# Kernel tuning notes

Hardware: AMD Instinct MI355X
Metric: run time of the kernel (lower is better)

The kernel has to match this reference:

```python
import jax, jax.numpy as jnp
import numpy as np
import math

N_HEADS = 32
N_KV_HEADS = 8
MAX_SEQ_LEN = 2048


def _rope_cos_sin(seq_len, head_dim, dtype):
    # precompute_freqs_cis: theta=10000, positions 0..seq_len-1 (note: NOT offset by start_pos, faithful to source)
    inv_freq = 1.0 / (10000.0 ** (jnp.arange(0, head_dim, 2, dtype=jnp.float32) / head_dim))
    t = jnp.arange(seq_len, dtype=jnp.float32)
    angles = jnp.outer(t, inv_freq)  # [S, hd/2]
    return jnp.cos(angles).astype(dtype), jnp.sin(angles).astype(dtype)


def _apply_rope(x, cos, sin):
    # x: [B, S, H, hd]; rotate consecutive pairs (llama complex convention)
    B, S, H, hd = x.shape
    xr = x.reshape(B, S, H, hd // 2, 2)
    x1, x2 = xr[..., 0], xr[..., 1]
    c = cos[None, :, None, :]
    s = sin[None, :, None, :]
    o1 = x1 * c - x2 * s
    o2 = x1 * s + x2 * c
    return jnp.stack([o1, o2], axis=-1).reshape(B, S, H, hd)


def setup_inputs() -> dict:
    key = jax.random.key(0)
    ks = jax.random.split(key, 5)
    dim = 4096
    B, S = 1, 2048
    sd = 1.0 / math.sqrt(dim)
    return {
        "x": jax.random.normal(ks[0], (B, S, dim), dtype=jnp.float32),
        "wq": jax.random.normal(ks[1], (4096, 4096), dtype=jnp.float32) * sd,
        "wk": jax.random.normal(ks[2], (1024, 4096), dtype=jnp.float32) * sd,
        "wv": jax.random.normal(ks[3], (1024, 4096), dtype=jnp.float32) * sd,
        "wo": jax.random.normal(ks[4], (4096, 4096), dtype=jnp.float32) * sd,
        "start_pos": 0,
    }


def reference(x, wq, wk, wv, wo, start_pos):
    B, S, D = x.shape
    Hq, Hkv = N_HEADS, N_KV_HEADS
    hd = D // Hq
    n_rep = Hq // Hkv

    xq = (x @ wq.T).reshape(B, S, Hq, hd)
    xk = (x @ wk.T).reshape(B, S, Hkv, hd)
    xv = (x @ wv.T).reshape(B, S, Hkv, hd)

    cos, sin = _rope_cos_sin(S, hd, x.dtype)
    xq = _apply_rope(xq, cos, sin)
    xk = _apply_rope(xk, cos, sin)

    # KV cache append + read back [:, :start_pos+S] (start_pos is a static Python int)
    cache_k = jnp.zeros((B, MAX_SEQ_LEN, Hkv, hd), dtype=x.dtype)
    cache_v = jnp.zeros((B, MAX_SEQ_LEN, Hkv, hd), dtype=x.dtype)
    cache_k = jax.lax.dynamic_update_slice(cache_k, xk, (0, start_pos, 0, 0))
    cache_v = jax.lax.dynamic_update_slice(cache_v, xv, (0, start_pos, 0, 0))
    kv_len = start_pos + S
    keys = cache_k[:, :kv_len]    # [B, K, Hkv, hd]
    values = cache_v[:, :kv_len]

    # GQA repeat_kv: [B, K, Hkv, hd] -> [B, K, Hq, hd]
    keys = jnp.broadcast_to(keys[:, :, :, None, :], (B, kv_len, Hkv, n_rep, hd)).reshape(B, kv_len, Hq, hd)
    values = jnp.broadcast_to(values[:, :, :, None, :], (B, kv_len, Hkv, n_rep, hd)).reshape(B, kv_len, Hq, hd)

    scale = 1.0 / math.sqrt(hd)
    scores = jnp.einsum('bqhd,bkhd->bhqk', xq, keys) * scale  # [B, Hq, S, K]
    # NOTE: source applies NO causal mask — faithful reproduction
    attn = jax.nn.softmax(scores, axis=-1)
    out = jnp.einsum('bhqk,bkhd->bqhd', attn, values).reshape(B, S, Hq * hd)
    return out @ wo.T
```

## Files before the change

### kernel.cpp

```cpp
#include <hip/hip_runtime.h>
#include <hip/hip_bf16.h>

typedef __bf16 bf16_t;
typedef _Float16 f16_t;
typedef unsigned int uint;
typedef __attribute__((ext_vector_type(8))) __bf16 bf16x8;
typedef __attribute__((ext_vector_type(4))) __bf16 bf16x4;
typedef __attribute__((ext_vector_type(8))) _Float16 f16x8;
typedef __attribute__((ext_vector_type(4))) _Float16 f16x4;
typedef __attribute__((ext_vector_type(4))) float f32x4;
typedef __attribute__((ext_vector_type(16))) float f32x16;

__global__ __launch_bounds__(256) void repack_x16(const float* __restrict__ src,
                                                  uint16_t* __restrict__ dh)
{
    const int p  = blockIdx.y;
    const int kb = blockIdx.x;
    const int tid = threadIdx.x;
    const int rr = tid >> 3;
    const int k4 = tid & 7;
    const int slot = k4 >> 1;
    const int so   = (k4 & 1) * 4;
    uint16_t* bh = dh + ((size_t)p * 128 + kb) * 4096;
    #pragma unroll
    for (int it = 0; it < 4; ++it) {
        const int r = it * 32 + rr;
        const float4 v = *reinterpret_cast<const float4*>(
            &src[((size_t)p * 128 + r) * 4096 + kb * 32 + k4 * 4]);
        float f[4] = {v.x, v.y, v.z, v.w};
        f16x4 h;
        #pragma unroll
        for (int e = 0; e < 4; ++e) h[e] = (f16_t)f[e];
        const int pos = r * 32 + ((slot ^ ((r >> 1) & 3)) << 3) + so;
        *reinterpret_cast<f16x4*>(&bh[pos]) = h;
    }
}

__global__ __launch_bounds__(256) void repack_w96_16(const float* __restrict__ wq,
                                                     const float* __restrict__ wk,
                                                     const float* __restrict__ wv,
                                                     uint16_t* __restrict__ dst)
{
    const int kb  = blockIdx.x;
    const int pan = blockIdx.y;
    const int tid = threadIdx.x;
    const int k4 = tid & 7;
    const int slot = k4 >> 1;
    const int so   = (k4 & 1) * 4;
    uint16_t* bh = dst + ((size_t)pan * 128 + kb) * 3072;
    #pragma unroll
    for (int it = 0; it < 3; ++it) {
        const int r = it * 32 + (tid >> 3);
        const int n = pan * 96 + r;
        const float* srow = (n < 4096) ? (wq + (size_t)n * 4096)
                          : (n < 5120) ? (wk + (size_t)(n - 4096) * 4096)
                                       : (wv + (size_t)(n - 5120) * 4096);
        const float4 v = *reinterpret_cast<const float4*>(srow + kb * 32 + k4 * 4);
        float f[4] = {v.x, v.y, v.z, v.w};
        f16x4 h;
        #pragma unroll
        for (int e = 0; e < 4; ++e) h[e] = (f16_t)f[e];
        const int pos = r * 32 + ((slot ^ ((r >> 1) & 3)) << 3) + so;
        *reinterpret_cast<f16x4*>(&bh[pos]) = h;
    }
}

__global__ __launch_bounds__(256) void repack_h16(const float* __restrict__ src,
                                                  uint16_t* __restrict__ dh)
{
    const int p  = blockIdx.y;
    const int kb = blockIdx.x;
    const int tid = threadIdx.x;
    const int rr = tid >> 3;
    const int k4 = tid & 7;
    const int slot = k4 >> 1;
    const int so   = (k4 & 1) * 4;
    uint16_t* bh = dh + ((size_t)p * 128 + kb) * 4096;
    #pragma unroll
    for (int it = 0; it < 4; ++it) {
        const int r = it * 32 + rr;
        const float4 v = *reinterpret_cast<const float4*>(
            &src[((size_t)p * 128 + r) * 4096 + kb * 32 + k4 * 4]);
        float f[4] = {v.x, v.y, v.z, v.w};
        f16x4 h;
        #pragma unroll
        for (int e = 0; e < 4; ++e) h[e] = (f16_t)f[e];
        const int pos = r * 32 + ((slot ^ ((r >> 1) & 3)) << 3) + so;
        *reinterpret_cast<f16x4*>(&bh[pos]) = h;
    }
}

__global__ __launch_bounds__(512) void gemm_qkv7(const uint16_t* __restrict__ xh,
                                                 const uint16_t* __restrict__ wqkv,
                                                 float* __restrict__ xq,
                                                 float* __restrict__ xk,
                                                 float* __restrict__ xv)
{
    __shared__ char lds[3][28672];

    const int bid = blockIdx.x;
    const int swz = (bid & 7) * 32 + (bid >> 3);
    const int by = swz >> 5;
    const int bx = swz & 31;
    const int tid = threadIdx.x;
    const int w = tid >> 6, lane = tid & 63;
    const int wm = w >> 2, wn = w & 3;
    const int fr = lane & 15, s4 = lane >> 4;

    const int cw = (w < 4) ? 4 : 3;
    const uint16_t* sp[4];
    int dof[4];
    int stridec[4];
    #pragma unroll
    for (int i = 0; i < 4; ++i) {
        const int c = w + 8 * i;
        if (c < 16) {
            sp[i] = xh + (size_t)(2 * by + (c >> 3)) * 524288 + (c & 7) * 512 + lane * 8;
            dof[i] = c * 1024;
            stridec[i] = 4096;
        } else {
            const int cb = (c - 16) % 12;
            sp[i] = wqkv + (size_t)(bx * 2 + (cb >= 6 ? 1 : 0)) * 393216 + (cb % 6) * 512 + lane * 8;
            dof[i] = 16384 + cb * 1024;
            stridec[i] = 3072;
        }
    }

    f32x4 acc[8][3] = {};

    #pragma unroll
    for (int i = 0; i < 4; ++i)
        if (i < cw)
            __builtin_amdgcn_global_load_lds(
                (const __attribute__((address_space(1))) void*)(sp[i]),
                (__attribute__((address_space(3))) void*)(&lds[0][0] + dof[i]), 16, 0, 0);
    #pragma unroll
    for (int i = 0; i < 4; ++i)
        if (i < cw)
            __builtin_amdgcn_global_load_lds(
                (const __attribute__((address_space(1))) void*)(sp[i] + stridec[i]),
                (__attribute__((address_space(3))) void*)(&lds[1][0] + dof[i]), 16, 0, 0);
    if (w < 4) asm volatile("s_waitcnt vmcnt(4)" ::: "memory");
    else       asm volatile("s_waitcnt vmcnt(3)" ::: "memory");
    __builtin_amdgcn_s_barrier();
    __builtin_amdgcn_sched_barrier(0);

    int cur = 0;
    for (int t = 0; t < 128; ++t) {
        if (t + 2 < 128) {
            int nb = cur + 2; if (nb >= 3) nb -= 3;
            #pragma unroll
            for (int i = 0; i < 4; ++i)
                if (i < cw)
                    __builtin_amdgcn_global_load_lds(
                        (const __attribute__((address_space(1))) void*)(sp[i] + (size_t)(t + 2) * stridec[i]),
                        (__attribute__((address_space(3))) void*)(&lds[nb][0] + dof[i]), 16, 0, 0);
        }
        const char* b = &lds[cur][0];

        f16x8 fb[3];
        #pragma unroll
        for (int j = 0; j < 3; ++j) {
            const int cbp = wn * 48 + j * 16 + fr;
            const int pan = (cbp >= 96) ? 1 : 0;
            const int rb = cbp - pan * 96;
            fb[j] = *reinterpret_cast<const f16x8*>(b + 16384 + pan * 6144 + rb * 64 + ((s4 ^ ((rb >> 1) & 3)) << 4));
        }
        #pragma unroll
        for (int p = 0; p < 4; ++p) {
            f16x8 fh[2];
            #pragma unroll
            for (int f = 0; f < 2; ++f) {
                const int rl = wm * 128 + p * 32 + f * 16 + fr;
                fh[f] = *reinterpret_cast<const f16x8*>(b + rl * 64 + ((s4 ^ ((rl >> 1) & 3)) << 4));
            }
            __builtin_amdgcn_s_setprio(1);
            #pragma unroll
            for (int f = 0; f < 2; ++f)
                #pragma unroll
                for (int j = 0; j < 3; ++j)
                    acc[p * 2 + f][j] = __builtin_amdgcn_mfma_f32_16x16x32_f16(fh[f], fb[j], acc[p * 2 + f][j], 0, 0, 0);
            __builtin_amdgcn_s_setprio(0);
        }
        if (t + 2 < 128) {
            if (w < 4) asm volatile("s_waitcnt vmcnt(4)" ::: "memory");
            else       asm volatile("s_waitcnt vmcnt(3)" ::: "memory");
        } else {
            asm volatile("s_waitcnt vmcnt(0)" ::: "memory");
        }
        __builtin_amdgcn_s_barrier();
        __builtin_amdgcn_sched_barrier(0);
        if (++cur == 3) cur = 0;
    }

    const int r0 = by * 256 + wm * 128 + s4 * 4;
    const int c0 = bx * 192 + wn * 48 + fr;
    #pragma unroll
    for (int ri = 0; ri < 8; ++ri)
        #pragma unroll
        for (int j = 0; j < 3; ++j) {
            const int col = c0 + j * 16;
            #pragma unroll
            for (int rr = 0; rr < 4; ++rr) {
                const int row = r0 + ri * 16 + rr;
                if (col < 4096)      xq[(size_t)row * 4096 + col] = acc[ri][j][rr];
                else if (col < 5120) xk[(size_t)row * 1024 + (col - 4096)] = acc[ri][j][rr];
                else                 xv[(size_t)row * 1024 + (col - 5120)] = acc[ri][j][rr];
            }
        }
}

__global__ __launch_bounds__(512) void gemm_out7(const uint16_t* __restrict__ aoh,
                                                 const uint16_t* __restrict__ woh,
                                                 float* __restrict__ out)
{
    __shared__ char lds[3][24576];

    const int bid = blockIdx.x;
    const int swz = (bid & 7) * 32 + (bid >> 3);
    const int by = swz >> 5;
    const int bx = swz & 31;
    const int tid = threadIdx.x;
    const int w = tid >> 6, lane = tid & 63;
    const int wm = w >> 2, wn = w & 3;
    const int fr = lane & 15, s4 = lane >> 4;

    const uint16_t* sp[3];
    int dof[3];
    #pragma unroll
    for (int i = 0; i < 3; ++i) {
        const int c = w + 8 * i;
        if (c < 16) {
            sp[i]  = aoh + (size_t)(2 * by + (c >> 3)) * 524288 + (c & 7) * 512 + lane * 8;
            dof[i] = c * 1024;
        } else {
            sp[i]  = woh + (size_t)bx * 524288 + (c - 16) * 512 + lane * 8;
            dof[i] = 16384 + (c - 16) * 1024;
        }
    }

    f32x4 acc[8][2] = {};

    #pragma unroll
    for (int i = 0; i < 3; ++i)
        __builtin_amdgcn_global_load_lds(
            (const __attribute__((address_space(1))) void*)(sp[i]),
            (__attribute__((address_space(3))) void*)(&lds[0][0] + dof[i]), 16, 0, 0);
    #pragma unroll
    for (int i = 0; i < 3; ++i)
        __builtin_amdgcn_global_load_lds(
            (const __attribute__((address_space(1))) void*)(sp[i] + 4096),
            (__attribute__((address_space(3))) void*)(&lds[1][0] + dof[i]), 16, 0, 0);
    asm volatile("s_waitcnt vmcnt(3)" ::: "memory");
    __builtin_amdgcn_s_barrier();
    __builtin_amdgcn_sched_barrier(0);

    int cur = 0;
    for (int t = 0; t < 128; ++t) {
        if (t + 2 < 128) {
            int nb = cur + 2; if (nb >= 3) nb -= 3;
            #pragma unroll
            for (int i = 0; i < 3; ++i)
                __builtin_amdgcn_global_load_lds(
                    (const __attribute__((address_space(1))) void*)(sp[i] + (size_t)(t + 2) * 4096),
                    (__attribute__((address_space(3))) void*)(&lds[nb][0] + dof[i]), 16, 0, 0);
        }
        const char* b = &lds[cur][0];

        f16x8 fb[2];
        #pragma unroll
        for (int j = 0; j < 2; ++j) {
            const int cbp = wn * 32 + j * 16 + fr;
            fb[j] = *reinterpret_cast<const f16x8*>(b + 16384 + cbp * 64 + ((s4 ^ ((cbp >> 1) & 3)) << 4));
        }
        #pragma unroll
        for (int p = 0; p < 4; ++p) {
            f16x8 fh[2];
            #pragma unroll
            for (int f = 0; f < 2; ++f) {
                const int rl = p * 32 + f * 16 + fr;
                fh[f] = *reinterpret_cast<const f16x8*>(b + wm * 8192 + rl * 64 + ((s4 ^ ((rl >> 1) & 3)) << 4));
            }
            __builtin_amdgcn_s_setprio(1);
            #pragma unroll
            for (int f = 0; f < 2; ++f)
                #pragma unroll
                for (int j = 0; j < 2; ++j)
                    acc[p * 2 + f][j] = __builtin_amdgcn_mfma_f32_16x16x32_f16(fh[f], fb[j], acc[p * 2 + f][j], 0, 0, 0);
            __builtin_amdgcn_s_setprio(0);
        }
        if (t + 2 < 128) asm volatile("s_waitcnt vmcnt(3)" ::: "memory");
        else             asm volatile("s_waitcnt vmcnt(0)" ::: "memory");
        __builtin_amdgcn_s_barrier();
        __builtin_amdgcn_sched_barrier(0);
        if (++cur == 3) cur = 0;
    }

    const int r0 = by * 256 + wm * 128 + s4 * 4;
    const int c0 = bx * 128 + wn * 32 + fr;
    #pragma unroll
    for (int ri = 0; ri < 8; ++ri)
        #pragma unroll
        for (int j = 0; j < 2; ++j)
            #pragma unroll
            for (int rr = 0; rr < 4; ++rr)
                out[(size_t)(r0 + ri * 16 + rr) * 4096 + c0 + j * 16] = acc[ri][j][rr];
}

__global__ __launch_bounds__(256) void rope_k(float* __restrict__ xq, float* __restrict__ xk)
{
    const int idx = blockIdx.x * 256 + threadIdx.x;
    const int TOTQ = 2048 * 32 * 64;
    int s, j;
    float* base;
    bool isq = idx < TOTQ;
    if (isq) {
        s = idx >> 11;
        const int rem = idx & 2047;
        j = rem & 63;
        base = xq + (size_t)s * 4096 + (rem >> 6) * 128 + 2 * j;
    } else {
        const int i2 = idx - TOTQ;
        s = i2 >> 9;
        const int rem = i2 & 511;
        j = rem & 63;
        base = xk + (size_t)s * 1024 + (rem >> 6) * 128 + 2 * j;
    }
    const float invf = exp2f(-(float)j * (13.287712379549449f / 64.0f));
    const float ang = (float)s * invf;
    float sn, cs;
    sincosf(ang, &sn, &cs);
    float2 v = *reinterpret_cast<float2*>(base);
    float2 r;
    r.x = v.x * cs - v.y * sn;
    r.y = v.x * sn + v.y * cs;
    if (isq) { r.x *= 0.08838834764831845f; r.y *= 0.08838834764831845f; }
    *reinterpret_cast<float2*>(base) = r;
}

__global__ __launch_bounds__(256) void conv_kv(const float* __restrict__ xk,
                                               const float* __restrict__ xv,
                                               uint16_t* __restrict__ kvg)
{
    __shared__ float V[32][129];
    const int t = blockIdx.x;
    const int h = blockIdx.y;
    const int tid = threadIdx.x;
    uint16_t* tile = kvg + ((size_t)(h * 64 + t)) * 12288;

    #pragma unroll
    for (int i = 0; i < 4; ++i) {
        int v = i * 256 + tid;
        int row = v >> 5, c4 = (v & 31) * 4;
        *reinterpret_cast<float4*>(&V[row][c4]) =
            *reinterpret_cast<const float4*>(&xv[(size_t)(t * 32 + row) * 1024 + h * 128 + c4]);
    }

    {
        const int r = tid >> 3;
        const int d0 = (tid & 7) * 16;
        float f[16];
        const float* kr = &xk[(size_t)(t * 32 + r) * 1024 + h * 128 + d0];
        *reinterpret_cast<float4*>(&f[0])  = *reinterpret_cast<const float4*>(kr);
        *reinterpret_cast<float4*>(&f[4])  = *reinterpret_cast<const float4*>(kr + 4);
        *reinterpret_cast<float4*>(&f[8])  = *reinterpret_cast<const float4*>(kr + 8);
        *reinterpret_cast<float4*>(&f[12]) = *reinterpret_cast<const float4*>(kr + 12);
        #pragma unroll
        for (int cc = 0; cc < 2; ++cc) {
            bf16x8 hv, lv;
            #pragma unroll
            for (int e = 0; e < 8; ++e) {
                float x = f[cc * 8 + e];
                bf16_t hb = (bf16_t)x;
                hv[e] = hb;
                lv[e] = (bf16_t)(x - (float)hb);
            }
            const int c = (d0 >> 3) + cc;
            const int pos = r * 128 + ((c ^ (r & 15)) << 3);
            *reinterpret_cast<bf16x8*>(&tile[pos]) = hv;
            *reinterpret_cast<bf16x8*>(&tile[4096 + pos]) = lv;
        }
    }
    __syncthreads();
    {
        const int d = tid >> 1;
        const int k0 = (tid & 1) * 16;
        float g[16];
        #pragma unroll
        for (int j = 0; j < 16; ++j) g[j] = V[k0 + j][d];
        #pragma unroll
        for (int cc = 0; cc < 2; ++cc) {
            bf16x8 hv;
            #pragma unroll
            for (int e = 0; e < 8; ++e) hv[e] = (bf16_t)g[cc * 8 + e];
            const int c = (k0 >> 3) + cc;
            const int pos = d * 32 + ((c ^ (d & 3)) << 3);
            *reinterpret_cast<bf16x8*>(&tile[8192 + pos]) = hv;
        }
    }
}

__device__ __forceinline__ uint cvtpk(float lo, float hi) {
    uint r;
    asm("v_cvt_pk_bf16_f32 %0, %1, %2" : "=v"(r) : "v"(lo), "v"(hi));
    return r;
}
__device__ __forceinline__ void permswap(uint& a, uint& b) {
    asm("v_permlane32_swap_b32 %0, %1" : "+v"(a), "+v"(b));
}
__device__ __forceinline__ bf16x8 pack4(uint w0, uint w1, uint w2, uint w3) {
    union { uint u[4]; bf16x8 v; } t;
    t.u[0] = w0; t.u[1] = w1; t.u[2] = w2; t.u[3] = w3;
    return t.v;
}

__global__ __launch_bounds__(512, 2) void attn_mfma(const float* __restrict__ xq,
                                                    const uint16_t* __restrict__ kvg,
                                                    uint16_t* __restrict__ aoh)
{
    __shared__ char lds[2][24576];

    const int b = blockIdx.x;
    const int kvh = b & 7;
    const int r = b >> 3;
    const int h = kvh * 4 + (r & 3);
    const int q0 = (r >> 2) * 256;
    const int tid = threadIdx.x;
    const int w = tid >> 6;
    const int lane = tid & 63;
    const int ln31 = lane & 31;
    const int hi = lane >> 5;

    const int q = q0 + w * 32 + ln31;
    const float* qrow = xq + (size_t)q * 4096 + h * 128;
    bf16x8 Qh[8];
    #pragma unroll
    for (int ks = 0; ks < 8; ++ks) {
        float f[8];
        *reinterpret_cast<float4*>(&f[0]) = *reinterpret_cast<const float4*>(qrow + ks * 16 + hi * 8);
        *reinterpret_cast<float4*>(&f[4]) = *reinterpret_cast<const float4*>(qrow + ks * 16 + hi * 8 + 4);
        #pragma unroll
        for (int e = 0; e < 8; ++e) Qh[ks][e] = (bf16_t)f[e];
    }

    const char* gkv = (const char*)kvg + (size_t)kvh * 64 * 24576;

    f32x16 oacc[4] = {{}, {}, {}, {}};
    float m = -3.0e38f, l = 0.f;

    {
        #pragma unroll
        for (int i = 0; i < 3; ++i) {
            const int chunk = i * 8 + w;
            __builtin_amdgcn_global_load_lds(
                (const __attribute__((address_space(1))) void*)(gkv + chunk * 1024 + lane * 16),
                (__attribute__((address_space(3))) void*)(&lds[0][chunk * 1024]),
                16, 0, 0);
        }
    }

    for (int t = 0; t < 64; ++t) {
        __syncthreads();
        if (t + 1 < 64) {
            const char* g = gkv + (size_t)(t + 1) * 24576;
            const int buf = (t + 1) & 1;
            #pragma unroll
            for (int i = 0; i < 3; ++i) {
                const int chunk = i * 8 + w;
                __builtin_amdgcn_global_load_lds(
                    (const __attribute__((address_space(1))) void*)(g + chunk * 1024 + lane * 16),
                    (__attribute__((address_space(3))) void*)(&lds[buf][chunk * 1024]),
                    16, 0, 0);
            }
        }
        const int cur = t & 1;
        const char* Kh = lds[cur];
        const char* Kl = lds[cur] + 8192;
        const char* Vh = lds[cur] + 16384;

        f32x16 s0 = {}, s1 = {};
        __builtin_amdgcn_s_setprio(1);
        #pragma unroll
        for (int ks = 0; ks < 8; ++ks) {
            const int byt = ln31 * 256 + ((ks * 32 + hi * 16) ^ ((ln31 & 15) << 4));
            bf16x8 ah = *reinterpret_cast<const bf16x8*>(Kh + byt);
            bf16x8 al = *reinterpret_cast<const bf16x8*>(Kl + byt);
            s0 = __builtin_amdgcn_mfma_f32_32x32x16_bf16(ah, Qh[ks], s0, 0, 0, 0);
            s1 = __builtin_amdgcn_mfma_f32_32x32x16_bf16(al, Qh[ks], s1, 0, 0, 0);
        }
        __builtin_amdgcn_s_setprio(0);
        f32x16 s = s0 + s1;

        float pmax = s[0];
        #pragma unroll
        for (int jj = 1; jj < 16; ++jj) pmax = fmaxf(pmax, s[jj]);
        pmax = fmaxf(pmax, __shfl_xor(pmax, 32));
        if (!__all(pmax - m <= 8.0f)) {
            const float mnew = fmaxf(m, pmax);
            const float corr = __expf(m - mnew);
            l *= corr;
            #pragma unroll
            for (int dt = 0; dt < 4; ++dt) oacc[dt] *= corr;
            m = mnew;
        }
        float psum = 0.f;
        #pragma unroll
        for (int jj = 0; jj < 16; ++jj) {
            float pv = __expf(s[jj] - m);
            s[jj] = pv;
            psum += pv;
        }
        psum += __shfl_xor(psum, 32);
        l += psum;

        #pragma unroll
        for (int ks = 0; ks < 2; ++ks) {
            const int b0 = ks * 8;
            uint wa = cvtpk(s[b0 + 0], s[b0 + 1]);
            uint wb = cvtpk(s[b0 + 2], s[b0 + 3]);
            uint wc = cvtpk(s[b0 + 4], s[b0 + 5]);
            uint wd = cvtpk(s[b0 + 6], s[b0 + 7]);
            permswap(wa, wc); permswap(wb, wd);
            bf16x8 Pf = pack4(wa, wb, wc, wd);
            __builtin_amdgcn_s_setprio(1);
            #pragma unroll
            for (int dt = 0; dt < 4; ++dt) {
                const int row = dt * 32 + ln31;
                const int byt = row * 64 + ((ks * 32 + hi * 16) ^ ((row & 3) << 4));
                bf16x8 vh = *reinterpret_cast<const bf16x8*>(Vh + byt);
                oacc[dt] = __builtin_amdgcn_mfma_f32_32x32x16_bf16(vh, Pf, oacc[dt], 0, 0, 0);
            }
            __builtin_amdgcn_s_setprio(0);
        }
    }

    const float invl = 1.0f / l;
    const int p   = q >> 7;
    const int rr_ = q & 127;
    const int rsw = (rr_ >> 1) & 3;
    #pragma unroll
    for (int dt = 0; dt < 4; ++dt) {
        const int kb = h * 4 + dt;
        uint16_t* bh = aoh + ((size_t)p * 128 + kb) * 4096;
        #pragma unroll
        for (int g4 = 0; g4 < 4; ++g4) {
            f16x4 hv;
            #pragma unroll
            for (int e = 0; e < 4; ++e)
                hv[e] = (f16_t)(oacc[dt][g4 * 4 + e] * invl);
            const int pos = rr_ * 32 + ((g4 ^ rsw) << 3) + 4 * hi;
            *reinterpret_cast<f16x4*>(&bh[pos]) = hv;
        }
    }
}

extern "C" void kernel_launch(void* const* d_in, const int* in_sizes, int n_in,
                              void* d_out, int out_size, void* d_ws, size_t ws_size,
                              hipStream_t stream)
{
    const float* x  = (const float*)d_in[0];
    const float* wq = (const float*)d_in[1];
    const float* wk = (const float*)d_in[2];
    const float* wv = (const float*)d_in[3];
    const float* wo = (const float*)d_in[4];
    float* out = (float*)d_out;

    float* ws = (float*)d_ws;
    float*    xq   = ws;
    uint16_t* kvg  = (uint16_t*)(ws + 8388608);
    float*    xk   = ws + 12582912;
    float*    xv   = ws + 14680064;
    uint16_t* aoh  = (uint16_t*)(ws + 12582912);
    uint16_t* xh   = (uint16_t*)(ws + 20971520);
    uint16_t* wqkv = (uint16_t*)(ws + 29360128);
    uint16_t* woh  = (uint16_t*)(ws + 41943040);

    dim3 blk(256);
    repack_x16   <<<dim3(128, 16), blk, 0, stream>>>(x, xh);
    repack_w96_16<<<dim3(128, 64), blk, 0, stream>>>(wq, wk, wv, wqkv);
    gemm_qkv7    <<<dim3(256), dim3(512), 0, stream>>>(xh, wqkv, xq, xk, xv);
    repack_h16   <<<dim3(128, 32), blk, 0, stream>>>(wo, woh);
    rope_k       <<<dim3(20480), blk, 0, stream>>>(xq, xk);
    conv_kv      <<<dim3(64, 8), blk, 0, stream>>>(xk, xv, kvg);
    attn_mfma    <<<dim3(256), dim3(512), 0, stream>>>(xq, kvg, aoh);
    gemm_out7    <<<dim3(256), dim3(512), 0, stream>>>(aoh, woh, out);
}
```

Baseline: 395.8 us.

## Use single f16 K in attention and double-buffer GEMMs with K=64 stages

The attention kernel stops splitting K into bf16 hi/lo parts and stores K and V as a single f16 copy. This halves the QK MFMAs and cuts the KV tile from 24KB to 16KB, at the cost of lower precision in the attention scores. Both GEMM kernels change from a 3-stage pipeline with 32-wide K steps to a 2-stage pipeline with 64-wide K steps and larger LDS buffers. That halves the number of barriers, but each step now waits for vmcnt(0), which may expose load latency.

```diff
diff --git a/kernel.cpp b/kernel.cpp
--- a/kernel.cpp
+++ b/kernel.cpp
@@ -1,11 +1,8 @@
 #include <hip/hip_runtime.h>
 #include <hip/hip_bf16.h>
 
-typedef __bf16 bf16_t;
 typedef _Float16 f16_t;
 typedef unsigned int uint;
-typedef __attribute__((ext_vector_type(8))) __bf16 bf16x8;
-typedef __attribute__((ext_vector_type(4))) __bf16 bf16x4;
 typedef __attribute__((ext_vector_type(8))) _Float16 f16x8;
 typedef __attribute__((ext_vector_type(4))) _Float16 f16x4;
 typedef __attribute__((ext_vector_type(4))) float f32x4;
@@ -90,13 +87,13 @@
     }
 }
 
-__global__ __launch_bounds__(512) void gemm_qkv7(const uint16_t* __restrict__ xh,
+__global__ __launch_bounds__(512) void gemm_qkv8(const uint16_t* __restrict__ xh,
                                                  const uint16_t* __restrict__ wqkv,
                                                  float* __restrict__ xq,
                                                  float* __restrict__ xk,
                                                  float* __restrict__ xv)
 {
-    __shared__ char lds[3][28672];
+    __shared__ char lds[2][57344];
 
     const int bid = blockIdx.x;
     const int swz = (bid & 7) * 32 + (bid >> 3);
@@ -107,90 +104,79 @@
     const int wm = w >> 2, wn = w & 3;
     const int fr = lane & 15, s4 = lane >> 4;
 
-    const int cw = (w < 4) ? 4 : 3;
-    const uint16_t* sp[4];
-    int dof[4];
-    int stridec[4];
-    #pragma unroll
-    for (int i = 0; i < 4; ++i) {
+    const uint16_t* sp[7];
+    int dof[7];
+    int stridec[7];
+    #pragma unroll
+    for (int i = 0; i < 7; ++i) {
         const int c = w + 8 * i;
-        if (c < 16) {
-            sp[i] = xh + (size_t)(2 * by + (c >> 3)) * 524288 + (c & 7) * 512 + lane * 8;
+        if (c < 32) {
+            const int pan = c >> 4, sub = c & 15;
+            sp[i] = xh + (size_t)(2 * by + pan) * 524288 + sub * 512 + lane * 8;
             dof[i] = c * 1024;
-            stridec[i] = 4096;
+            stridec[i] = 8192;
         } else {
-            const int cb = (c - 16) % 12;
-            sp[i] = wqkv + (size_t)(bx * 2 + (cb >= 6 ? 1 : 0)) * 393216 + (cb % 6) * 512 + lane * 8;
-            dof[i] = 16384 + cb * 1024;
-            stridec[i] = 3072;
+            const int cb = c - 32;
+            const int pan = cb / 12, sub = cb % 12;
+            sp[i] = wqkv + (size_t)(bx * 2 + pan) * 393216 + sub * 512 + lane * 8;
+            dof[i] = 32768 + cb * 1024;
+            stridec[i] = 6144;
         }
     }
 
     f32x4 acc[8][3] = {};
 
     #pragma unroll
-    for (int i = 0; i < 4; ++i)
-        if (i < cw)
-            __builtin_amdgcn_global_load_lds(
-                (const __attribute__((address_space(1))) void*)(sp[i]),
-                (__attribute__((address_space(3))) void*)(&lds[0][0] + dof[i]), 16, 0, 0);
-    #pragma unroll
-    for (int i = 0; i < 4; ++i)
-        if (i < cw)
-            __builtin_amdgcn_global_load_lds(
-                (const __attribute__((address_space(1))) void*)(sp[i] + stridec[i]),
-                (__attribute__((address_space(3))) void*)(&lds[1][0] + dof[i]), 16, 0, 0);
-    if (w < 4) asm volatile("s_waitcnt vmcnt(4)" ::: "memory");
-    else       asm volatile("s_waitcnt vmcnt(3)" ::: "memory");
+    for (int i = 0; i < 7; ++i)
+        __builtin_amdgcn_global_load_lds(
+            (const __attribute__((address_space(1))) void*)(sp[i]),
+            (__attribute__((address_space(3))) void*)(&lds[0][0] + dof[i]), 16, 0, 0);
+    asm volatile("s_waitcnt vmcnt(0)" ::: "memory");
     __builtin_amdgcn_s_barrier();
     __builtin_amdgcn_sched_barrier(0);
 
-    int cur = 0;
-    for (int t = 0; t < 128; ++t) {
-        if (t + 2 < 128) {
-            int nb = cur + 2; if (nb >= 3) nb -= 3;
-            #pragma unroll
-            for (int i = 0; i < 4; ++i)
-                if (i < cw)
-                    __builtin_amdgcn_global_load_lds(
-                        (const __attribute__((address_space(1))) void*)(sp[i] + (size_t)(t + 2) * stridec[i]),
-                        (__attribute__((address_space(3))) void*)(&lds[nb][0] + dof[i]), 16, 0, 0);
-        }
-        const char* b = &lds[cur][0];
-
-        f16x8 fb[3];
-        #pragma unroll
-        for (int j = 0; j < 3; ++j) {
-            const int cbp = wn * 48 + j * 16 + fr;
-            const int pan = (cbp >= 96) ? 1 : 0;
-            const int rb = cbp - pan * 96;
-            fb[j] = *reinterpret_cast<const f16x8*>(b + 16384 + pan * 6144 + rb * 64 + ((s4 ^ ((rb >> 1) & 3)) << 4));
-        }
-        #pragma unroll
-        for (int p = 0; p < 4; ++p) {
-            f16x8 fh[2];
-            #pragma unroll
-            for (int f = 0; f < 2; ++f) {
-                const int rl = wm * 128 + p * 32 + f * 16 + fr;
-                fh[f] = *reinterpret_cast<const f16x8*>(b + rl * 64 + ((s4 ^ ((rl >> 1) & 3)) << 4));
-            }
-            __builtin_amdgcn_s_setprio(1);
-            #pragma unroll
-            for (int f = 0; f < 2; ++f)
+    for (int t = 0; t < 64; ++t) {
+        const char* b = &lds[t & 1][0];
+        if (t + 1 < 64) {
+            char* nb = &lds[(t + 1) & 1][0];
+            #pragma unroll
+            for (int i = 0; i < 7; ++i)
+                __builtin_amdgcn_global_load_lds(
+                    (const __attribute__((address_space(1))) void*)(sp[i] + (size_t)(t + 1) * stridec[i]),
+                    (__attribute__((address_space(3))) void*)(nb + dof[i]), 16, 0, 0);
+        }
+        #pragma unroll
+        for (int kk = 0; kk < 2; ++kk) {
+            f16x8 fb[3];
+            #pragma unroll
+            for (int j = 0; j < 3; ++j) {
+                const int cbp = wn * 48 + j * 16 + fr;
+                const int pan = (cbp >= 96) ? 1 : 0;
+                const int rb = cbp - pan * 96;
+                fb[j] = *reinterpret_cast<const f16x8*>(
+                    b + 32768 + pan * 12288 + kk * 6144 + rb * 64 + ((s4 ^ ((rb >> 1) & 3)) << 4));
+            }
+            #pragma unroll
+            for (int p = 0; p < 4; ++p) {
+                f16x8 fh[2];
                 #pragma unroll
-                for (int j = 0; j < 3; ++j)
-                    acc[p * 2 + f][j] = __builtin_amdgcn_mfma_f32_16x16x32_f16(fh[f], fb[j], acc[p * 2 + f][j], 0, 0, 0);
-            __builtin_amdgcn_s_setprio(0);
-        }
-        if (t + 2 < 128) {
-            if (w < 4) asm volatile("s_waitcnt vmcnt(4)" ::: "memory");
-            else       asm volatile("s_waitcnt vmcnt(3)" ::: "memory");
-        } else {
-            asm volatile("s_waitcnt vmcnt(0)" ::: "memory");
-        }
+                for (int f = 0; f < 2; ++f) {
+                    const int rloc = p * 32 + f * 16 + fr;
+                    fh[f] = *reinterpret_cast<const f16x8*>(
+                        b + wm * 16384 + kk * 8192 + rloc * 64 + ((s4 ^ ((rloc >> 1) & 3)) << 4));
+                }
+                __builtin_amdgcn_s_setprio(1);
+                #pragma unroll
+                for (int f = 0; f < 2; ++f)
+                    #pragma unroll
+                    for (int j = 0; j < 3; ++j)
+                        acc[p * 2 + f][j] = __builtin_amdgcn_mfma_f32_16x16x32_f16(fh[f], fb[j], acc[p * 2 + f][j], 0, 0, 0);
+                __builtin_amdgcn_s_setprio(0);
+            }
+        }
+        asm volatile("s_waitcnt vmcnt(0)" ::: "memory");
         __builtin_amdgcn_s_barrier();
         __builtin_amdgcn_sched_barrier(0);
-        if (++cur == 3) cur = 0;
     }
 
     const int r0 = by * 256 + wm * 128 + s4 * 4;
@@ -210,11 +196,11 @@
         }
 }
 
-__global__ __launch_bounds__(512) void gemm_out7(const uint16_t* __restrict__ aoh,
+__global__ __launch_bounds__(512) void gemm_out8(const uint16_t* __restrict__ aoh,
                                                  const uint16_t* __restrict__ woh,
                                                  float* __restrict__ out)
 {
-    __shared__ char lds[3][24576];
+    __shared__ char lds[2][49152];
 
     const int bid = blockIdx.x;
     const int swz = (bid & 7) * 32 + (bid >> 3);
@@ -225,75 +211,72 @@
     const int wm = w >> 2, wn = w & 3;
     const int fr = lane & 15, s4 = lane >> 4;
 
-    const uint16_t* sp[3];
-    int dof[3];
-    #pragma unroll
-    for (int i = 0; i < 3; ++i) {
+    const uint16_t* sp[6];
+    int dof[6];
+    #pragma unroll
+    for (int i = 0; i < 6; ++i) {
         const int c = w + 8 * i;
-        if (c < 16) {
-            sp[i]  = aoh + (size_t)(2 * by + (c >> 3)) * 524288 + (c & 7) * 512 + lane * 8;
+        if (c < 32) {
+            const int pan = c >> 4, sub = c & 15;
+            sp[i] = aoh + (size_t)(2 * by + pan) * 524288 + sub * 512 + lane * 8;
             dof[i] = c * 1024;
         } else {
-            sp[i]  = woh + (size_t)bx * 524288 + (c - 16) * 512 + lane * 8;
-            dof[i] = 16384 + (c - 16) * 1024;
+            sp[i] = woh + (size_t)bx * 524288 + (c - 32) * 512 + lane * 8;
+            dof[i] = 32768 + (c - 32) * 1024;
         }
     }
 
     f32x4 acc[8][2] = {};
 
     #pragma unroll
-    for (int i = 0; i < 3; ++i)
+    for (int i = 0; i < 6; ++i)
         __builtin_amdgcn_global_load_lds(
             (const __attribute__((address_space(1))) void*)(sp[i]),
             (__attribute__((address_space(3))) void*)(&lds[0][0] + dof[i]), 16, 0, 0);
-    #pragma unroll
-    for (int i = 0; i < 3; ++i)
-        __builtin_amdgcn_global_load_lds(
-            (const __attribute__((address_space(1))) void*)(sp[i] + 4096),
-            (__attribute__((address_space(3))) void*)(&lds[1][0] + dof[i]), 16, 0, 0);
-    asm volatile("s_waitcnt vmcnt(3)" ::: "memory");
+    asm volatile("s_waitcnt vmcnt(0)" ::: "memory");
     __builtin_amdgcn_s_barrier();
     __builtin_amdgcn_sched_barrier(0);
 
-    int cur = 0;
-    for (int t = 0; t < 128; ++t) {
-        if (t + 2 < 128) {
-            int nb = cur + 2; if (nb >= 3) nb -= 3;
-            #pragma unroll
-            for (int i = 0; i < 3; ++i)
+    for (int t = 0; t < 64; ++t) {
+        const char* b = &lds[t & 1][0];
+        if (t + 1 < 64) {
+            char* nb = &lds[(t + 1) & 1][0];
+            #pragma unroll
+            for (int i = 0; i < 6; ++i)
                 __builtin_amdgcn_global_load_lds(
-                    (const __attribute__((address_space(1))) void*)(sp[i] + (size_t)(t + 2) * 4096),
-                    (__attribute__((address_space(3))) void*)(&lds[nb][0] + dof[i]), 16, 0, 0);
-        }
-        const char* b = &lds[cur][0];
-
-        f16x8 fb[2];
-        #pragma unroll
-        for (int j = 0; j < 2; ++j) {
-            const int cbp = wn * 32 + j * 16 + fr;
-            fb[j] = *reinterpret_cast<const f16x8*>(b + 16384 + cbp * 64 + ((s4 ^ ((cbp >> 1) & 3)) << 4));
-        }
-        #pragma unroll
-        for (int p = 0; p < 4; ++p) {
-            f16x8 fh[2];
-            #pragma unroll
-            for (int f = 0; f < 2; ++f) {
-                const int rl = p * 32 + f * 16 + fr;
-                fh[f] = *reinterpret_cast<const f16x8*>(b + wm * 8192 + rl * 64 + ((s4 ^ ((rl >> 1) & 3)) << 4));
-            }
-            __builtin_amdgcn_s_setprio(1);
-            #pragma unroll
-            for (int f = 0; f < 2; ++f)
+                    (const __attribute__((address_space(1))) void*)(sp[i] + (size_t)(t + 1) * 8192),
+                    (__attribute__((address_space(3))) void*)(nb + dof[i]), 16, 0, 0);
+        }
+        #pragma unroll
+        for (int kk = 0; kk < 2; ++kk) {
+            f16x8 fb[2];
+            #pragma unroll
+            for (int j = 0; j < 2; ++j) {
+                const int cbp = wn * 32 + j * 16 + fr;
+                fb[j] = *reinterpret_cast<const f16x8*>(
+                    b + 32768 + kk * 8192 + cbp * 64 + ((s4 ^ ((cbp >> 1) & 3)) << 4));
+            }
+            #pragma unroll
+            for (int p = 0; p < 4; ++p) {
+                f16x8 fh[2];
                 #pragma unroll
-                for (int j = 0; j < 2; ++j)
-                    acc[p * 2 + f][j] = __builtin_amdgcn_mfma_f32_16x16x32_f16(fh[f], fb[j], acc[p * 2 + f][j], 0, 0, 0);
-            __builtin_amdgcn_s_setprio(0);
-        }
-        if (t + 2 < 128) asm volatile("s_waitcnt vmcnt(3)" ::: "memory");
-        else             asm volatile("s_waitcnt vmcnt(0)" ::: "memory");
+                for (int f = 0; f < 2; ++f) {
+                    const int rloc = p * 32 + f * 16 + fr;
+                    fh[f] = *reinterpret_cast<const f16x8*>(
+                        b + wm * 16384 + kk * 8192 + rloc * 64 + ((s4 ^ ((rloc >> 1) & 3)) << 4));
+                }
+                __builtin_amdgcn_s_setprio(1);
+                #pragma unroll
+                for (int f = 0; f < 2; ++f)
+                    #pragma unroll
+                    for (int j = 0; j < 2; ++j)
+                        acc[p * 2 + f][j] = __builtin_amdgcn_mfma_f32_16x16x32_f16(fh[f], fb[j], acc[p * 2 + f][j], 0, 0, 0);
+                __builtin_amdgcn_s_setprio(0);
+            }
+        }
+        asm volatile("s_waitcnt vmcnt(0)" ::: "memory");
         __builtin_amdgcn_s_barrier();
         __builtin_amdgcn_sched_barrier(0);
-        if (++cur == 3) cur = 0;
     }
 
     const int r0 = by * 256 + wm * 128 + s4 * 4;
@@ -346,7 +329,7 @@
     const int t = blockIdx.x;
     const int h = blockIdx.y;
     const int tid = threadIdx.x;
-    uint16_t* tile = kvg + ((size_t)(h * 64 + t)) * 12288;
+    uint16_t* tile = kvg + ((size_t)(h * 64 + t)) * 8192;
 
     #pragma unroll
     for (int i = 0; i < 4; ++i) {
@@ -367,18 +350,12 @@
         *reinterpret_cast<float4*>(&f[12]) = *reinterpret_cast<const float4*>(kr + 12);
         #pragma unroll
         for (int cc = 0; cc < 2; ++cc) {
-            bf16x8 hv, lv;
-            #pragma unroll
-            for (int e = 0; e < 8; ++e) {
-                float x = f[cc * 8 + e];
-                bf16_t hb = (bf16_t)x;
-                hv[e] = hb;
-                lv[e] = (bf16_t)(x - (float)hb);
-            }
+            f16x8 hv;
+            #pragma unroll
+            for (int e = 0; e < 8; ++e) hv[e] = (f16_t)f[cc * 8 + e];
             const int c = (d0 >> 3) + cc;
             const int pos = r * 128 + ((c ^ (r & 15)) << 3);
-            *reinterpret_cast<bf16x8*>(&tile[pos]) = hv;
-            *reinterpret_cast<bf16x8*>(&tile[4096 + pos]) = lv;
+            *reinterpret_cast<f16x8*>(&tile[pos]) = hv;
         }
     }
     __syncthreads();
@@ -390,26 +367,26 @@
         for (int j = 0; j < 16; ++j) g[j] = V[k0 + j][d];
         #pragma unroll
         for (int cc = 0; cc < 2; ++cc) {
-            bf16x8 hv;
-            #pragma unroll
-            for (int e = 0; e < 8; ++e) hv[e] = (bf16_t)g[cc * 8 + e];
+            f16x8 hv;
+            #pragma unroll
+            for (int e = 0; e < 8; ++e) hv[e] = (f16_t)g[cc * 8 + e];
             const int c = (k0 >> 3) + cc;
-            const int pos = d * 32 + ((c ^ (d & 3)) << 3);
-            *reinterpret_cast<bf16x8*>(&tile[8192 + pos]) = hv;
-        }
-    }
-}
-
-__device__ __forceinline__ uint cvtpk(float lo, float hi) {
+            const int pos = 4096 + d * 32 + ((c ^ (d & 3)) << 3);
+            *reinterpret_cast<f16x8*>(&tile[pos]) = hv;
+        }
+    }
+}
+
+__device__ __forceinline__ uint cvtpkh(float lo, float hi) {
     uint r;
-    asm("v_cvt_pk_bf16_f32 %0, %1, %2" : "=v"(r) : "v"(lo), "v"(hi));
+    asm("v_cvt_pkrtz_f16_f32 %0, %1, %2" : "=v"(r) : "v"(lo), "v"(hi));
     return r;
 }
 __device__ __forceinline__ void permswap(uint& a, uint& b) {
     asm("v_permlane32_swap_b32 %0, %1" : "+v"(a), "+v"(b));
 }
-__device__ __forceinline__ bf16x8 pack4(uint w0, uint w1, uint w2, uint w3) {
-    union { uint u[4]; bf16x8 v; } t;
+__device__ __forceinline__ f16x8 pack4h(uint w0, uint w1, uint w2, uint w3) {
+    union { uint u[4]; f16x8 v; } t;
     t.u[0] = w0; t.u[1] = w1; t.u[2] = w2; t.u[3] = w3;
     return t.v;
 }
@@ -418,7 +395,7 @@
                                                     const uint16_t* __restrict__ kvg,
                                                     uint16_t* __restrict__ aoh)
 {
-    __shared__ char lds[2][24576];
+    __shared__ char lds[2][16384];
 
     const int b = blockIdx.x;
     const int kvh = b & 7;
@@ -433,24 +410,24 @@
 
     const int q = q0 + w * 32 + ln31;
     const float* qrow = xq + (size_t)q * 4096 + h * 128;
-    bf16x8 Qh[8];
+    f16x8 Qh[8];
     #pragma unroll
     for (int ks = 0; ks < 8; ++ks) {
         float f[8];
         *reinterpret_cast<float4*>(&f[0]) = *reinterpret_cast<const float4*>(qrow + ks * 16 + hi * 8);
         *reinterpret_cast<float4*>(&f[4]) = *reinterpret_cast<const float4*>(qrow + ks * 16 + hi * 8 + 4);
         #pragma unroll
-        for (int e = 0; e < 8; ++e) Qh[ks][e] = (bf16_t)f[e];
-    }
-
-    const char* gkv = (const char*)kvg + (size_t)kvh * 64 * 24576;
+        for (int e = 0; e < 8; ++e) Qh[ks][e] = (f16_t)f[e];
+    }
+
+    const char* gkv = (const char*)kvg + (size_t)kvh * 64 * 16384;
 
     f32x16 oacc[4] = {{}, {}, {}, {}};
     float m = -3.0e38f, l = 0.f;
 
     {
         #pragma unroll
-        for (int i = 0; i < 3; ++i) {
+        for (int i = 0; i < 2; ++i) {
             const int chunk = i * 8 + w;
             __builtin_amdgcn_global_load_lds(
                 (const __attribute__((address_space(1))) void*)(gkv + chunk * 1024 + lane * 16),
@@ -462,10 +439,10 @@
     for (int t = 0; t < 64; ++t) {
         __syncthreads();
         if (t + 1 < 64) {
-            const char* g = gkv + (size_t)(t + 1) * 24576;
+            const char* g = gkv + (size_t)(t + 1) * 16384;
             const int buf = (t + 1) & 1;
             #pragma unroll
-            for (int i = 0; i < 3; ++i) {
+            for (int i = 0; i < 2; ++i) {
                 const int chunk = i * 8 + w;
                 __builtin_amdgcn_global_load_lds(
                     (const __attribute__((address_space(1))) void*)(g + chunk * 1024 + lane * 16),
@@ -474,19 +451,17 @@
             }
         }
         const int cur = t & 1;
-        const char* Kh = lds[cur];
-        const char* Kl = lds[cur] + 8192;
-        const char* Vh = lds[cur] + 16384;
+        const char* Kf = lds[cur];
+        const char* Vf = lds[cur] + 8192;
 
         f32x16 s0 = {}, s1 = {};
         __builtin_amdgcn_s_setprio(1);
         #pragma unroll
         for (int ks = 0; ks < 8; ++ks) {
             const int byt = ln31 * 256 + ((ks * 32 + hi * 16) ^ ((ln31 & 15) << 4));
-            bf16x8 ah = *reinterpret_cast<const bf16x8*>(Kh + byt);
-            bf16x8 al = *reinterpret_cast<const bf16x8*>(Kl + byt);
-            s0 = __builtin_amdgcn_mfma_f32_32x32x16_bf16(ah, Qh[ks], s0, 0, 0, 0);
-            s1 = __builtin_amdgcn_mfma_f32_32x32x16_bf16(al, Qh[ks], s1, 0, 0, 0);
+            f16x8 a = *reinterpret_cast<const f16x8*>(Kf + byt);
+            if (ks & 1) s1 = __builtin_amdgcn_mfma_f32_32x32x16_f16(a, Qh[ks], s1, 0, 0, 0);
+            else        s0 = __builtin_amdgcn_mfma_f32_32x32x16_f16(a, Qh[ks], s0, 0, 0, 0);
         }
         __builtin_amdgcn_s_setprio(0);
         f32x16 s = s0 + s1;
@@ -516,19 +491,19 @@
         #pragma unroll
         for (int ks = 0; ks < 2; ++ks) {
             const int b0 = ks * 8;
-            uint wa = cvtpk(s[b0 + 0], s[b0 + 1]);
-            uint wb = cvtpk(s[b0 + 2], s[b0 + 3]);
-            uint wc = cvtpk(s[b0 + 4], s[b0 + 5]);
-            uint wd = cvtpk(s[b0 + 6], s[b0 + 7]);
+            uint wa = cvtpkh(s[b0 + 0], s[b0 + 1]);
+            uint wb = cvtpkh(s[b0 + 2], s[b0 + 3]);
+            uint wc = cvtpkh(s[b0 + 4], s[b0 + 5]);
+            uint wd = cvtpkh(s[b0 + 6], s[b0 + 7]);
             permswap(wa, wc); permswap(wb, wd);
-            bf16x8 Pf = pack4(wa, wb, wc, wd);
+            f16x8 Pf = pack4h(wa, wb, wc, wd);
             __builtin_amdgcn_s_setprio(1);
             #pragma unroll
             for (int dt = 0; dt < 4; ++dt) {
                 const int row = dt * 32 + ln31;
                 const int byt = row * 64 + ((ks * 32 + hi * 16) ^ ((row & 3) << 4));
-                bf16x8 vh = *reinterpret_cast<const bf16x8*>(Vh + byt);
-                oacc[dt] = __builtin_amdgcn_mfma_f32_32x32x16_bf16(vh, Pf, oacc[dt], 0, 0, 0);
+                f16x8 vh = *reinterpret_cast<const f16x8*>(Vf + byt);
+                oacc[dt] = __builtin_amdgcn_mfma_f32_32x32x16_f16(vh, Pf, oacc[dt], 0, 0, 0);
             }
             __builtin_amdgcn_s_setprio(0);
         }
@@ -578,10 +553,10 @@
     dim3 blk(256);
     repack_x16   <<<dim3(128, 16), blk, 0, stream>>>(x, xh);
     repack_w96_16<<<dim3(128, 64), blk, 0, stream>>>(wq, wk, wv, wqkv);
-    gemm_qkv7    <<<dim3(256), dim3(512), 0, stream>>>(xh, wqkv, xq, xk, xv);
+    gemm_qkv8    <<<dim3(256), dim3(512), 0, stream>>>(xh, wqkv, xq, xk, xv);
     repack_h16   <<<dim3(128, 32), blk, 0, stream>>>(wo, woh);
     rope_k       <<<dim3(20480), blk, 0, stream>>>(xq, xk);
     conv_kv      <<<dim3(64, 8), blk, 0, stream>>>(xk, xv, kvg);
     attn_mfma    <<<dim3(256), dim3(512), 0, stream>>>(xq, kvg, aoh);
-    gemm_out7    <<<dim3(256), dim3(512), 0, stream>>>(aoh, woh, out);
-}
+    gemm_out8    <<<dim3(256), dim3(512), 0, stream>>>(aoh, woh, out);
+}
```

Result: faster. 371.8 us (-6.1%).
